# Kernel optimization log

Hardware: AMD Instinct MI355X
Metric: run time of the kernel (lower is better)

## Reference

```python
import jax, jax.numpy as jnp
import numpy as np

D_MODEL = 1024
N_HEAD = 16
HEAD_DIM = D_MODEL // N_HEAD


def setup_inputs() -> dict:
    key = jax.random.key(0)
    ks = jax.random.split(key, 12)
    B, S, D = 4, 2048, D_MODEL
    s = 1.0 / np.sqrt(D)
    inp = {
        "query": jax.random.normal(ks[0], (B, S, D), jnp.float32),
        "key": jax.random.normal(ks[1], (B, S, D), jnp.float32),
        "value": jax.random.normal(ks[2], (B, S, D), jnp.float32),
        "mask": jnp.ones((B, 1, 1, S), jnp.int32),
        "Wq": jax.random.normal(ks[3], (D, D), jnp.float32) * s,
        "bq": jnp.zeros((D,), jnp.float32),
        "Wk": jax.random.normal(ks[4], (D, D), jnp.float32) * s,
        "bk": jnp.zeros((D,), jnp.float32),
        "Wv": jax.random.normal(ks[5], (D, D), jnp.float32) * s,
        "bv": jnp.zeros((D,), jnp.float32),
        "Wo": jax.random.normal(ks[6], (D, D), jnp.float32) * s,
        "bo": jnp.zeros((D,), jnp.float32),
    }
    return inp


def _split_heads(x, W, b):
    # x: [B, S, D] -> [B, H, S, Dh]
    B, S, _ = x.shape
    out = x @ W + b
    return out.reshape(B, S, N_HEAD, HEAD_DIM).transpose(0, 2, 1, 3)


def reference(query, key, value, mask, Wq, bq, Wk, bk, Wv, bv, Wo, bo):
    B, S, D = query.shape
    q = _split_heads(query, Wq, bq)
    k = _split_heads(key, Wk, bk)
    v = _split_heads(value, Wv, bv)
    scale = 1.0 / jnp.sqrt(jnp.asarray(HEAD_DIM, q.dtype))
    scores = jnp.einsum("bhqd,bhkd->bhqk", q, k) * scale  # [B,H,S,S]
    scores = jnp.where(mask == 0, jnp.asarray(-1e9, scores.dtype), scores)
    attn = jax.nn.softmax(scores, axis=-1)  # dropout is identity in eval mode
    out = jnp.einsum("bhqk,bhkd->bhqd", attn, v)
    out = out.transpose(0, 2, 1, 3).reshape(B, S, D)
    return out @ Wo + bo
```

## Files before the change

kernel.cpp:

```cpp
#include <hip/hip_runtime.h>


typedef float  f32x4  __attribute__((ext_vector_type(4)));
typedef float  f32x16 __attribute__((ext_vector_type(16)));
typedef short  s16x8  __attribute__((ext_vector_type(8)));
typedef unsigned short u16x4 __attribute__((ext_vector_type(4)));

#define DEV static __device__ __forceinline__

DEV unsigned short f2bf(float f) {
  unsigned u = __float_as_uint(f);
  u += 0x7fffu + ((u >> 16) & 1u);
  return (unsigned short)(u >> 16);
}

DEV unsigned cvtpk(float lo, float hi) {
  unsigned r;
  asm("v_cvt_pk_bf16_f32 %0, %1, %2" : "=v"(r) : "v"(lo), "v"(hi));
  return r;
}

DEV void gld_lds16(const void* g, void* l) {
  __builtin_amdgcn_global_load_lds(
      (const __attribute__((address_space(1))) unsigned int*)g,
      (__attribute__((address_space(3))) unsigned int*)l, 16, 0, 0);
}

__global__ __launch_bounds__(256) void wtrans_kernel(
    const float* __restrict__ W0, const float* __restrict__ W1,
    const float* __restrict__ W2, const float* __restrict__ W3,
    unsigned short* __restrict__ T0, unsigned short* __restrict__ T1,
    unsigned short* __restrict__ T2, unsigned short* __restrict__ T3)
{
  __shared__ float tile[64][65];
  const float* W; unsigned short* T;
  switch (blockIdx.z) {
    case 0: W = W0; T = T0; break;
    case 1: W = W1; T = T1; break;
    case 2: W = W2; T = T2; break;
    default: W = W3; T = T3; break;
  }
  const int bi = blockIdx.x, bj = blockIdx.y;
  const int t = threadIdx.x;
  const int c4 = (t & 15) * 4, rr = t >> 4;
  #pragma unroll
  for (int j = 0; j < 4; j++) {
    int r = j * 16 + rr;
    float4 v = *(const float4*)(W + (size_t)(bi * 64 + r) * 1024 + bj * 64 + c4);
    tile[r][c4 + 0] = v.x; tile[r][c4 + 1] = v.y;
    tile[r][c4 + 2] = v.z; tile[r][c4 + 3] = v.w;
  }
  __syncthreads();
  #pragma unroll
  for (int j = 0; j < 4; j++) {
    int n = j * 16 + rr;
    uint2 p;
    p.x = cvtpk(tile[c4 + 0][n], tile[c4 + 1][n]);
    p.y = cvtpk(tile[c4 + 2][n], tile[c4 + 3][n]);
    *(uint2*)(T + (size_t)(bj * 64 + n) * 1024 + bi * 64 + c4) = p;
  }
}

__global__ __launch_bounds__(256) void gemm_qkv_kernel(
    const float* __restrict__ Aq, const float* __restrict__ Ak, const float* __restrict__ Av,
    const unsigned short* __restrict__ Btq, const unsigned short* __restrict__ Btk,
    const unsigned short* __restrict__ Btv,
    const float* __restrict__ pbq, const float* __restrict__ pbk, const float* __restrict__ pbv,
    unsigned short* __restrict__ Qp, unsigned short* __restrict__ Kp,
    unsigned short* __restrict__ Vtg)
{
  const int z = blockIdx.z;
  const float* A  = (z == 0) ? Aq : (z == 1) ? Ak : Av;
  const unsigned short* Bt = (z == 0) ? Btq : (z == 1) ? Btk : Btv;
  const float* bias = (z == 0) ? pbq : (z == 1) ? pbk : pbv;
  unsigned short* outp = (z == 0) ? Qp : (z == 1) ? Kp : Vtg;
  const float scale = (z == 0) ? 0.18033688011112042f : 1.0f;
  const int epi = (z == 2) ? 1 : 0;

  const int tid = threadIdx.x;
  const int lane = tid & 63, w = tid >> 6;
  const int wm = w >> 1, wn = w & 1;
  const int H = blockIdx.y * 8 + blockIdx.x;
  const int L = (H & 7) * 64 + (H >> 3);
  const int m0 = (L >> 3) * 128, n0 = (L & 7) * 128;
  __shared__ __align__(16) char sA[8192];
  __shared__ __align__(16) char sB[8192];

  f32x4 acc[4][4];
  #pragma unroll
  for (int i = 0; i < 4; i++)
    #pragma unroll
    for (int j = 0; j < 4; j++)
      #pragma unroll
      for (int r = 0; r < 4; r++) acc[i][j][r] = 0.f;

  const int arow = tid >> 3;
  const int akl  = (tid & 7) * 4;
  const int brow = lane >> 2;
  const int bkl  = (lane & 3) * 8;

  for (int kt = 0; kt < 32; kt++) {
    const int k0 = kt * 32;
    #pragma unroll
    for (int j = 0; j < 4; j++) {
      int row = arow + j * 32;
      float4 v = *(const float4*)(A + (size_t)(m0 + row) * 1024 + k0 + akl);
      uint2 p; p.x = cvtpk(v.x, v.y); p.y = cvtpk(v.z, v.w);
      *(uint2*)(sA + row * 64 + akl * 2) = p;
    }
    #pragma unroll
    for (int j = 0; j < 2; j++) {
      int row = (w * 2 + j) * 16 + brow;
      gld_lds16(Bt + (size_t)(n0 + row) * 1024 + k0 + bkl, sB + (w * 2 + j) * 1024);
    }
    __syncthreads();
    s16x8 aF[4], bF[4];
    #pragma unroll
    for (int i = 0; i < 4; i++)
      aF[i] = *(const s16x8*)(sA + (wm * 64 + i * 16 + (lane & 15)) * 64 + (lane >> 4) * 16);
    #pragma unroll
    for (int i = 0; i < 4; i++)
      bF[i] = *(const s16x8*)(sB + (wn * 64 + i * 16 + (lane & 15)) * 64 + (lane >> 4) * 16);
    #pragma unroll
    for (int mi = 0; mi < 4; mi++)
      #pragma unroll
      for (int ni = 0; ni < 4; ni++)
        acc[mi][ni] = __builtin_amdgcn_mfma_f32_16x16x32_bf16(aF[mi], bF[ni], acc[mi][ni], 0, 0, 0);
    __syncthreads();
  }

  #pragma unroll
  for (int ni = 0; ni < 4; ni++) {
    const int gn = n0 + wn * 64 + ni * 16 + (lane & 15);
    const float bval = bias[gn];
    const int h_ = gn >> 6, d_ = gn & 63;
    #pragma unroll
    for (int mi = 0; mi < 4; mi++) {
      const int gm = m0 + wm * 64 + mi * 16 + (lane >> 4) * 4;
      const int b_ = gm >> 11, s_ = gm & 2047;
      f32x4 a = acc[mi][ni];
      if (epi == 0) {
        #pragma unroll
        for (int r = 0; r < 4; r++)
          outp[((size_t)(b_ * 16 + h_) * 2048 + (s_ + r)) * 64 + d_] =
              f2bf((a[r] + bval) * scale);
      } else {
        uint2 p;
        p.x = cvtpk(a[0] + bval, a[1] + bval);
        p.y = cvtpk(a[2] + bval, a[3] + bval);
        *(uint2*)(outp + ((size_t)(b_ * 16 + h_) * 64 + d_) * 2048 + s_) = p;
      }
    }
  }
}

__global__ __launch_bounds__(256) void attn_kernel(
    const unsigned short* __restrict__ Qp, const unsigned short* __restrict__ Kp,
    const unsigned short* __restrict__ Vtg, const int* __restrict__ mask,
    unsigned short* __restrict__ ctx)
{
  constexpr int S = 2048;
  const int tid = threadIdx.x;
  const int lane = tid & 63, w = tid >> 6;
  const int hi = lane >> 5, q31 = lane & 31;
  const int H = blockIdx.y * 16 + blockIdx.x;
  const int L = (H & 7) * 128 + (H >> 3);
  const int qb = L & 15, bh = L >> 4;
  const int b = bh >> 4, h = bh & 15;
  const int q0 = qb * 128;
  __shared__ __align__(16) char KsB[2][8192];
  __shared__ __align__(16) char VsB[2][8192];

  const int qrow = q0 + w * 32 + q31;
  const unsigned short* qptr = Qp + ((size_t)bh * S + qrow) * 64;
  s16x8 qf[4];
  #pragma unroll
  for (int ks = 0; ks < 4; ks++) qf[ks] = *(const s16x8*)(qptr + ks * 16 + hi * 8);

  f32x16 o[2];
  #pragma unroll
  for (int d = 0; d < 2; d++)
    #pragma unroll
    for (int i = 0; i < 16; i++) o[d][i] = 0.f;
  float m_run = -1e30f, l_run = 0.f;

  const int* mrow = mask + b * S;
  bool all1 = true;
  for (int t = 0; t < 32; t++) all1 &= (mrow[t * 64 + lane] != 0);
  const bool fullmask = (__ballot(all1) == ~0ull);

  auto STAGE = [&](int bsel, int kv0) {
    #pragma unroll
    for (int j = 0; j < 2; j++) {
      const int cb = (w * 2 + j) * 1024;
      const int oo = cb + lane * 16;
      const int row = oo >> 7;
      const int c = oo & 127;
      const int srcc = (c ^ ((row & 7) << 4)) >> 1;
      gld_lds16(Kp  + ((size_t)bh * S  + kv0 + row) * 64 + srcc, &KsB[bsel][cb]);
      gld_lds16(Vtg + ((size_t)bh * 64 + row) * S + kv0  + srcc, &VsB[bsel][cb]);
    }
  };

  auto TILE = [&](const char* Ks, const char* Vts, int kv0) {
    f32x16 sc[2];
    #pragma unroll
    for (int kvf = 0; kvf < 2; kvf++)
      #pragma unroll
      for (int i = 0; i < 16; i++) sc[kvf][i] = 0.f;

    __builtin_amdgcn_s_setprio(1);
    #pragma unroll
    for (int kvf = 0; kvf < 2; kvf++) {
      const int krow = kvf * 32 + q31;
      const int sw = (krow & 7) << 4;
      #pragma unroll
      for (int ks = 0; ks < 4; ks++) {
        s16x8 kf = *(const s16x8*)(Ks + krow * 128 + ((ks * 32 + hi * 16) ^ sw));
        sc[kvf] = __builtin_amdgcn_mfma_f32_32x32x16_bf16(kf, qf[ks], sc[kvf], 0, 0, 0);
      }
    }
    __builtin_amdgcn_s_setprio(0);

    if (!fullmask) {
      const unsigned long long mv = __ballot(mrow[kv0 + lane] != 0);
      if (mv != ~0ull) {
        #pragma unroll
        for (int kvf = 0; kvf < 2; kvf++)
          #pragma unroll
          for (int r = 0; r < 16; r++) {
            int kvp = kvf * 32 + (r & 3) + 8 * (r >> 2) + 4 * hi;
            if (!((mv >> kvp) & 1ull)) sc[kvf][r] = -1e30f;
          }
      }
    }

    float mx[4] = {-1e30f, -1e30f, -1e30f, -1e30f};
    #pragma unroll
    for (int kvf = 0; kvf < 2; kvf++)
      #pragma unroll
      for (int r = 0; r < 16; r++) mx[r & 3] = fmaxf(mx[r & 3], sc[kvf][r]);
    float mloc = fmaxf(fmaxf(mx[0], mx[1]), fmaxf(mx[2], mx[3]));
    mloc = fmaxf(mloc, __shfl_xor(mloc, 32));

    const float mnew = fmaxf(m_run, mloc);
    const float alpha = __builtin_amdgcn_exp2f(m_run - mnew);
    m_run = mnew;
    #pragma unroll
    for (int d = 0; d < 2; d++)
      #pragma unroll
      for (int i = 0; i < 16; i++) o[d][i] *= alpha;

    float ps[4] = {0.f, 0.f, 0.f, 0.f};
    #pragma unroll
    for (int kvf = 0; kvf < 2; kvf++)
      #pragma unroll
      for (int r = 0; r < 16; r++) {
        float p = __builtin_amdgcn_exp2f(sc[kvf][r] - m_run);
        sc[kvf][r] = p;
        ps[r & 3] += p;
      }
    float psum = (ps[0] + ps[1]) + (ps[2] + ps[3]);
    psum += __shfl_xor(psum, 32);
    l_run = l_run * alpha + psum;

    s16x8 pa[4];
    #pragma unroll
    for (int ks = 0; ks < 4; ks++) {
      const int kvf = ks >> 1, base = (ks & 1) * 8;
      unsigned a0 = cvtpk(sc[kvf][base + 0], sc[kvf][base + 1]);
      unsigned a1 = cvtpk(sc[kvf][base + 2], sc[kvf][base + 3]);
      unsigned b0 = cvtpk(sc[kvf][base + 4], sc[kvf][base + 5]);
      unsigned b1 = cvtpk(sc[kvf][base + 6], sc[kvf][base + 7]);
      unsigned ax0 = __shfl_xor(a0, 32), ax1 = __shfl_xor(a1, 32);
      unsigned bx0 = __shfl_xor(b0, 32), bx1 = __shfl_xor(b1, 32);
      union { unsigned u[4]; s16x8 s; } cv;
      cv.u[0] = hi ? bx0 : a0;
      cv.u[1] = hi ? bx1 : a1;
      cv.u[2] = hi ? b0  : ax0;
      cv.u[3] = hi ? b1  : ax1;
      pa[ks] = cv.s;
    }

    __builtin_amdgcn_s_setprio(1);
    #pragma unroll
    for (int df = 0; df < 2; df++) {
      const int vrow = df * 32 + q31;
      const int sw = (vrow & 7) << 4;
      #pragma unroll
      for (int ks = 0; ks < 4; ks++) {
        s16x8 vf = *(const s16x8*)(Vts + vrow * 128 + ((ks * 32 + hi * 16) ^ sw));
        o[df] = __builtin_amdgcn_mfma_f32_32x32x16_bf16(vf, pa[ks], o[df], 0, 0, 0);
      }
    }
    __builtin_amdgcn_s_setprio(0);
  };

  STAGE(0, 0);
  __syncthreads();
  for (int t = 0; t < 32; t += 2) {
    STAGE(1, (t + 1) * 64);
    TILE(KsB[0], VsB[0], t * 64);
    __syncthreads();
    if (t + 2 < 32) STAGE(0, (t + 2) * 64);
    TILE(KsB[1], VsB[1], (t + 1) * 64);
    __syncthreads();
  }

  const float inv = 1.0f / l_run;
  unsigned short* cp = ctx + ((size_t)(b * S + qrow)) * 1024 + h * 64;
  #pragma unroll
  for (int df = 0; df < 2; df++)
    #pragma unroll
    for (int rq = 0; rq < 4; rq++) {
      uint2 pw;
      pw.x = cvtpk(o[df][rq * 4 + 0] * inv, o[df][rq * 4 + 1] * inv);
      pw.y = cvtpk(o[df][rq * 4 + 2] * inv, o[df][rq * 4 + 3] * inv);
      *(uint2*)(cp + df * 32 + rq * 8 + hi * 4) = pw;
    }
}

__global__ __launch_bounds__(256) void gemm_out_kernel(
    const unsigned short* __restrict__ Actx, const unsigned short* __restrict__ Bt,
    const float* __restrict__ bias, float* __restrict__ outp)
{
  const int tid = threadIdx.x;
  const int lane = tid & 63, w = tid >> 6;
  const int wm = w >> 1, wn = w & 1;
  const int H = blockIdx.y * 8 + blockIdx.x;
  const int L = (H & 7) * 64 + (H >> 3);
  const int m0 = (L >> 3) * 128, n0 = (L & 7) * 128;
  __shared__ __align__(16) char sA[8192];
  __shared__ __align__(16) char sB[8192];

  f32x4 acc[4][4];
  #pragma unroll
  for (int i = 0; i < 4; i++)
    #pragma unroll
    for (int j = 0; j < 4; j++)
      #pragma unroll
      for (int r = 0; r < 4; r++) acc[i][j][r] = 0.f;

  const int brow = lane >> 2;
  const int bkl  = (lane & 3) * 8;

  for (int kt = 0; kt < 32; kt++) {
    const int k0 = kt * 32;
    #pragma unroll
    for (int j = 0; j < 2; j++) {
      int row = (w * 2 + j) * 16 + brow;
      gld_lds16(Actx + (size_t)(m0 + row) * 1024 + k0 + bkl, sA + (w * 2 + j) * 1024);
      gld_lds16(Bt   + (size_t)(n0 + row) * 1024 + k0 + bkl, sB + (w * 2 + j) * 1024);
    }
    __syncthreads();
    s16x8 aF[4], bF[4];
    #pragma unroll
    for (int i = 0; i < 4; i++)
      aF[i] = *(const s16x8*)(sA + (wm * 64 + i * 16 + (lane & 15)) * 64 + (lane >> 4) * 16);
    #pragma unroll
    for (int i = 0; i < 4; i++)
      bF[i] = *(const s16x8*)(sB + (wn * 64 + i * 16 + (lane & 15)) * 64 + (lane >> 4) * 16);
    #pragma unroll
    for (int mi = 0; mi < 4; mi++)
      #pragma unroll
      for (int ni = 0; ni < 4; ni++)
        acc[mi][ni] = __builtin_amdgcn_mfma_f32_16x16x32_bf16(aF[mi], bF[ni], acc[mi][ni], 0, 0, 0);
    __syncthreads();
  }

  #pragma unroll
  for (int ni = 0; ni < 4; ni++) {
    const int gn = n0 + wn * 64 + ni * 16 + (lane & 15);
    const float bval = bias[gn];
    #pragma unroll
    for (int mi = 0; mi < 4; mi++) {
      const int gm = m0 + wm * 64 + mi * 16 + (lane >> 4) * 4;
      #pragma unroll
      for (int r = 0; r < 4; r++)
        outp[(size_t)(gm + r) * 1024 + gn] = acc[mi][ni][r] + bval;
    }
  }
}

extern "C" void kernel_launch(void* const* d_in, const int* in_sizes, int n_in,
                              void* d_out, int out_size, void* d_ws, size_t ws_size,
                              hipStream_t stream)
{
  const float* query = (const float*)d_in[0];
  const float* key_  = (const float*)d_in[1];
  const float* value = (const float*)d_in[2];
  const int*   mask  = (const int*)d_in[3];
  const float* Wq = (const float*)d_in[4];
  const float* bq = (const float*)d_in[5];
  const float* Wk = (const float*)d_in[6];
  const float* bk = (const float*)d_in[7];
  const float* Wv = (const float*)d_in[8];
  const float* bv = (const float*)d_in[9];
  const float* Wo = (const float*)d_in[10];
  const float* bo = (const float*)d_in[11];
  float* out = (float*)d_out;

  unsigned short* Wtq = (unsigned short*)d_ws;
  unsigned short* Wtk = Wtq + (1u << 20);
  unsigned short* Wtv = Wtk + (1u << 20);
  unsigned short* Wto = Wtv + (1u << 20);
  unsigned short* Qp  = Wto + (1u << 20);
  unsigned short* Kp  = Qp  + (8u << 20);
  unsigned short* Vtg = Kp  + (8u << 20);
  unsigned short* ctx = Vtg + (8u << 20);

  wtrans_kernel<<<dim3(16, 16, 4), 256, 0, stream>>>(Wq, Wk, Wv, Wo, Wtq, Wtk, Wtv, Wto);
  gemm_qkv_kernel<<<dim3(8, 64, 3), 256, 0, stream>>>(query, key_, value,
                                                      Wtq, Wtk, Wtv, bq, bk, bv,
                                                      Qp, Kp, Vtg);
  attn_kernel<<<dim3(16, 64), 256, 0, stream>>>(Qp, Kp, Vtg, mask, ctx);
  gemm_out_kernel<<<dim3(8, 64), 256, 0, stream>>>(ctx, Wto, bo, out);
}
```

Baseline: 462.7 us.

## Load K/V fragments directly from global memory, dropping LDS double-buffer staging

```diff
diff --git a/kernel.cpp b/kernel.cpp
--- a/kernel.cpp
+++ b/kernel.cpp
@@ -168,14 +168,15 @@
   const int qb = L & 15, bh = L >> 4;
   const int b = bh >> 4, h = bh & 15;
   const int q0 = qb * 128;
-  __shared__ __align__(16) char KsB[2][8192];
-  __shared__ __align__(16) char VsB[2][8192];
 
   const int qrow = q0 + w * 32 + q31;
   const unsigned short* qptr = Qp + ((size_t)bh * S + qrow) * 64;
   s16x8 qf[4];
   #pragma unroll
   for (int ks = 0; ks < 4; ks++) qf[ks] = *(const s16x8*)(qptr + ks * 16 + hi * 8);
+
+  const unsigned short* kb = Kp  + (size_t)bh * S * 64 + q31 * 64 + hi * 8;
+  const unsigned short* vb = Vtg + (size_t)bh * 64 * S + q31 * S + hi * 8;
 
   f32x16 o[2];
   #pragma unroll
@@ -189,20 +190,9 @@
   for (int t = 0; t < 32; t++) all1 &= (mrow[t * 64 + lane] != 0);
   const bool fullmask = (__ballot(all1) == ~0ull);
 
-  auto STAGE = [&](int bsel, int kv0) {
-    #pragma unroll
-    for (int j = 0; j < 2; j++) {
-      const int cb = (w * 2 + j) * 1024;
-      const int oo = cb + lane * 16;
-      const int row = oo >> 7;
-      const int c = oo & 127;
-      const int srcc = (c ^ ((row & 7) << 4)) >> 1;
-      gld_lds16(Kp  + ((size_t)bh * S  + kv0 + row) * 64 + srcc, &KsB[bsel][cb]);
-      gld_lds16(Vtg + ((size_t)bh * 64 + row) * S + kv0  + srcc, &VsB[bsel][cb]);
-    }
-  };
-
-  auto TILE = [&](const char* Ks, const char* Vts, int kv0) {
+  for (int t = 0; t < 32; t++) {
+    const int kv0 = t * 64;
+
     f32x16 sc[2];
     #pragma unroll
     for (int kvf = 0; kvf < 2; kvf++)
@@ -212,12 +202,11 @@
     __builtin_amdgcn_s_setprio(1);
     #pragma unroll
     for (int kvf = 0; kvf < 2; kvf++) {
-      const int krow = kvf * 32 + q31;
-      const int sw = (krow & 7) << 4;
+      const unsigned short* kr = kb + (size_t)(kv0 + kvf * 32) * 64;
       #pragma unroll
       for (int ks = 0; ks < 4; ks++) {
-        s16x8 kf = *(const s16x8*)(Ks + krow * 128 + ((ks * 32 + hi * 16) ^ sw));
-        sc[kvf] = __builtin_amdgcn_mfma_f32_32x32x16_bf16(kf, qf[ks], sc[kvf], 0, 0, 0);
+        s16x8 kfr = *(const s16x8*)(kr + ks * 16);
+        sc[kvf] = __builtin_amdgcn_mfma_f32_32x32x16_bf16(kfr, qf[ks], sc[kvf], 0, 0, 0);
       }
     }
     __builtin_amdgcn_s_setprio(0);
@@ -285,26 +274,14 @@
     __builtin_amdgcn_s_setprio(1);
     #pragma unroll
     for (int df = 0; df < 2; df++) {
-      const int vrow = df * 32 + q31;
-      const int sw = (vrow & 7) << 4;
+      const unsigned short* vr = vb + (size_t)(df * 32) * S + kv0;
       #pragma unroll
       for (int ks = 0; ks < 4; ks++) {
-        s16x8 vf = *(const s16x8*)(Vts + vrow * 128 + ((ks * 32 + hi * 16) ^ sw));
-        o[df] = __builtin_amdgcn_mfma_f32_32x32x16_bf16(vf, pa[ks], o[df], 0, 0, 0);
+        s16x8 vfr = *(const s16x8*)(vr + ks * 16);
+        o[df] = __builtin_amdgcn_mfma_f32_32x32x16_bf16(vfr, pa[ks], o[df], 0, 0, 0);
       }
     }
     __builtin_amdgcn_s_setprio(0);
-  };
-
-  STAGE(0, 0);
-  __syncthreads();
-  for (int t = 0; t < 32; t += 2) {
-    STAGE(1, (t + 1) * 64);
-    TILE(KsB[0], VsB[0], t * 64);
-    __syncthreads();
-    if (t + 2 < 32) STAGE(0, (t + 2) * 64);
-    TILE(KsB[1], VsB[1], (t + 1) * 64);
-    __syncthreads();
   }
 
   const float inv = 1.0f / l_run;
```

Measured after the change: 520.1 us. 1.12x slower.

## Pre-convert QKV activations to bf16 and single-buffer attention K/V tiles

Applied to the files above, without the earlier changes.

```diff
diff --git a/kernel.cpp b/kernel.cpp
--- a/kernel.cpp
+++ b/kernel.cpp
@@ -61,8 +61,23 @@
   }
 }
 
+__global__ __launch_bounds__(256) void a2b_kernel(
+    const float* __restrict__ Aq, const float* __restrict__ Ak,
+    const float* __restrict__ Av, unsigned short* __restrict__ Xb)
+{
+  const int z = blockIdx.y;
+  const float* src = (z == 0) ? Aq : (z == 1) ? Ak : Av;
+  const size_t i = ((size_t)blockIdx.x * 256 + threadIdx.x) * 8;
+  float4 v0 = *(const float4*)(src + i);
+  float4 v1 = *(const float4*)(src + i + 4);
+  uint4 p;
+  p.x = cvtpk(v0.x, v0.y); p.y = cvtpk(v0.z, v0.w);
+  p.z = cvtpk(v1.x, v1.y); p.w = cvtpk(v1.z, v1.w);
+  *(uint4*)(Xb + (size_t)z * 8388608 + i) = p;
+}
+
 __global__ __launch_bounds__(256) void gemm_qkv_kernel(
-    const float* __restrict__ Aq, const float* __restrict__ Ak, const float* __restrict__ Av,
+    const unsigned short* __restrict__ Xb,
     const unsigned short* __restrict__ Btq, const unsigned short* __restrict__ Btk,
     const unsigned short* __restrict__ Btv,
     const float* __restrict__ pbq, const float* __restrict__ pbk, const float* __restrict__ pbv,
@@ -70,7 +85,7 @@
     unsigned short* __restrict__ Vtg)
 {
   const int z = blockIdx.z;
-  const float* A  = (z == 0) ? Aq : (z == 1) ? Ak : Av;
+  const unsigned short* A = Xb + (size_t)z * 8388608;
   const unsigned short* Bt = (z == 0) ? Btq : (z == 1) ? Btk : Btv;
   const float* bias = (z == 0) ? pbq : (z == 1) ? pbk : pbv;
   unsigned short* outp = (z == 0) ? Qp : (z == 1) ? Kp : Vtg;
@@ -94,23 +109,15 @@
       #pragma unroll
       for (int r = 0; r < 4; r++) acc[i][j][r] = 0.f;
 
-  const int arow = tid >> 3;
-  const int akl  = (tid & 7) * 4;
   const int brow = lane >> 2;
   const int bkl  = (lane & 3) * 8;
 
   for (int kt = 0; kt < 32; kt++) {
     const int k0 = kt * 32;
     #pragma unroll
-    for (int j = 0; j < 4; j++) {
-      int row = arow + j * 32;
-      float4 v = *(const float4*)(A + (size_t)(m0 + row) * 1024 + k0 + akl);
-      uint2 p; p.x = cvtpk(v.x, v.y); p.y = cvtpk(v.z, v.w);
-      *(uint2*)(sA + row * 64 + akl * 2) = p;
-    }
-    #pragma unroll
     for (int j = 0; j < 2; j++) {
       int row = (w * 2 + j) * 16 + brow;
+      gld_lds16(A  + (size_t)(m0 + row) * 1024 + k0 + bkl, sA + (w * 2 + j) * 1024);
       gld_lds16(Bt + (size_t)(n0 + row) * 1024 + k0 + bkl, sB + (w * 2 + j) * 1024);
     }
     __syncthreads();
@@ -168,8 +175,8 @@
   const int qb = L & 15, bh = L >> 4;
   const int b = bh >> 4, h = bh & 15;
   const int q0 = qb * 128;
-  __shared__ __align__(16) char KsB[2][8192];
-  __shared__ __align__(16) char VsB[2][8192];
+  __shared__ __align__(16) char Ks[8192];
+  __shared__ __align__(16) char Vts[8192];
 
   const int qrow = q0 + w * 32 + q31;
   const unsigned short* qptr = Qp + ((size_t)bh * S + qrow) * 64;
@@ -189,7 +196,8 @@
   for (int t = 0; t < 32; t++) all1 &= (mrow[t * 64 + lane] != 0);
   const bool fullmask = (__ballot(all1) == ~0ull);
 
-  auto STAGE = [&](int bsel, int kv0) {
+  for (int t = 0; t < 32; t++) {
+    const int kv0 = t * 64;
     #pragma unroll
     for (int j = 0; j < 2; j++) {
       const int cb = (w * 2 + j) * 1024;
@@ -197,12 +205,11 @@
       const int row = oo >> 7;
       const int c = oo & 127;
       const int srcc = (c ^ ((row & 7) << 4)) >> 1;
-      gld_lds16(Kp  + ((size_t)bh * S  + kv0 + row) * 64 + srcc, &KsB[bsel][cb]);
-      gld_lds16(Vtg + ((size_t)bh * 64 + row) * S + kv0  + srcc, &VsB[bsel][cb]);
-    }
-  };
-
-  auto TILE = [&](const char* Ks, const char* Vts, int kv0) {
+      gld_lds16(Kp  + ((size_t)bh * S  + kv0 + row) * 64 + srcc, Ks  + cb);
+      gld_lds16(Vtg + ((size_t)bh * 64 + row) * S + kv0  + srcc, Vts + cb);
+    }
+    __syncthreads();
+
     f32x16 sc[2];
     #pragma unroll
     for (int kvf = 0; kvf < 2; kvf++)
@@ -294,16 +301,6 @@
       }
     }
     __builtin_amdgcn_s_setprio(0);
-  };
-
-  STAGE(0, 0);
-  __syncthreads();
-  for (int t = 0; t < 32; t += 2) {
-    STAGE(1, (t + 1) * 64);
-    TILE(KsB[0], VsB[0], t * 64);
-    __syncthreads();
-    if (t + 2 < 32) STAGE(0, (t + 2) * 64);
-    TILE(KsB[1], VsB[1], (t + 1) * 64);
     __syncthreads();
   }
 
@@ -404,14 +401,15 @@
   unsigned short* Wtk = Wtq + (1u << 20);
   unsigned short* Wtv = Wtk + (1u << 20);
   unsigned short* Wto = Wtv + (1u << 20);
-  unsigned short* Qp  = Wto + (1u << 20);
+  unsigned short* Xb  = Wto + (1u << 20);
+  unsigned short* ctx = Xb;
+  unsigned short* Qp  = Xb  + (24u << 20);
   unsigned short* Kp  = Qp  + (8u << 20);
   unsigned short* Vtg = Kp  + (8u << 20);
-  unsigned short* ctx = Vtg + (8u << 20);
 
   wtrans_kernel<<<dim3(16, 16, 4), 256, 0, stream>>>(Wq, Wk, Wv, Wo, Wtq, Wtk, Wtv, Wto);
-  gemm_qkv_kernel<<<dim3(8, 64, 3), 256, 0, stream>>>(query, key_, value,
-                                                      Wtq, Wtk, Wtv, bq, bk, bv,
+  a2b_kernel<<<dim3(4096, 3), 256, 0, stream>>>(query, key_, value, Xb);
+  gemm_qkv_kernel<<<dim3(8, 64, 3), 256, 0, stream>>>(Xb, Wtq, Wtk, Wtv, bq, bk, bv,
                                                       Qp, Kp, Vtg);
   attn_kernel<<<dim3(16, 64), 256, 0, stream>>>(Qp, Kp, Vtg, mask, ctx);
   gemm_out_kernel<<<dim3(8, 64), 256, 0, stream>>>(ctx, Wto, bo, out);
```

Result: faster. 390.2 us (-15.7%).
